# Kernel optimization log

Measured on AMD Instinct MI355X. Metric: run time of the kernel, lower is better.

Reference implementation:

```python
import jax, jax.numpy as jnp
import numpy as np

WS = 11        # gaussian window size
SIGMA = 1.5    # gaussian sigma
L = 10.0       # val_range
SSIM_C1 = (0.01 * L) ** 2
SSIM_C2 = (0.03 * L) ** 2


def _window():
    g = jnp.exp(-((jnp.arange(WS) - WS // 2) ** 2) / (2.0 * SIGMA ** 2))
    g = g / g.sum()
    return jnp.outer(g, g).astype(jnp.float32)  # [11,11], sums to 1


def _blur(z, win):
    # depthwise 11x11 gaussian blur with VALID padding; z: [..., H, W]
    lead = z.shape[:-2]
    zf = z.reshape((-1, 1) + z.shape[-2:])
    out = jax.lax.conv_general_dilated(zf, win[None, None], (1, 1), 'VALID')
    return out.reshape(lead + out.shape[-2:])


def setup_inputs() -> dict:
    key = jax.random.key(0)
    ks = jax.random.split(key, 7)
    B, C, Fc, H, W = 8, 64, 3, 192, 192
    return {
        'x': jax.random.normal(ks[0], (B, C, H, W), jnp.float32),
        'x_feature': jax.random.normal(ks[1], (B, Fc, H, W), jnp.float32),
        'spatial_w': jax.random.normal(ks[2], (1, Fc, 3, 1), jnp.float32) * 0.1,
        'W1': jax.random.normal(ks[3], (C, C), jnp.float32) * 0.05,
        'b1': jnp.zeros((C,), jnp.float32),
        'W2': jax.random.normal(ks[4], (C, C), jnp.float32) * 0.05,
        'b2': jnp.zeros((C,), jnp.float32),
    }


def reference(x, x_feature, spatial_w, W1, b1, W2, b2):
    win = _window()
    # per-channel gaussian moments (computed once, reused across all pairs)
    mu_x = _blur(x, win)                         # [B,C,h,w]
    mu_f = _blur(x_feature, win)                 # [B,F,h,w]
    sig_x = _blur(x * x, win) - mu_x ** 2        # variance of x channels
    sig_f = _blur(x_feature * x_feature, win) - mu_f ** 2
    # all pairwise cross-covariances in one batched blur
    prod = x_feature[:, :, None] * x[:, None]    # [B,F,C,H,W]
    sig_fx = _blur(prod, win) - mu_f[:, :, None] * mu_x[:, None]
    v1 = 2.0 * sig_fx + SSIM_C2
    v2 = sig_f[:, :, None] + sig_x[:, None] + SSIM_C2
    num = (2.0 * mu_f[:, :, None] * mu_x[:, None] + SSIM_C1) * v1
    den = (mu_f[:, :, None] ** 2 + mu_x[:, None] ** 2 + SSIM_C1) * v2
    ssim_info = (num / den).mean(axis=(-2, -1))  # [B,F,C]
    # spatial gate: Conv2d(3,1,(3,1),padding=(1,0)) over [B,F,C,1]
    si4 = ssim_info[..., None]                   # [B,F,C,1]
    h = jax.lax.conv_general_dilated(si4, spatial_w, (1, 1), ((1, 1), (0, 0)))
    h = jax.nn.relu(h).reshape(x.shape[0], -1)   # [B,C]
    h = jax.nn.relu(h @ W1.T + b1) @ W2.T + b2
    return jax.nn.sigmoid(h), ssim_info
```

## Files before the change

kernel.cpp:

```cpp
#include <hip/hip_runtime.h>
#include <math.h>

#define HW 192
#define OW 182
#define NPIX (OW*OW)
#define SSIM_C1 0.01f
#define SSIM_C2 0.09f

#define Gk0 0.0010283835f
#define Gk1 0.0075987615f
#define Gk2 0.0360007700f
#define Gk3 0.1093608000f
#define Gk4 0.2130055400f
#define Gk5 0.2660117000f

typedef float v2f __attribute__((ext_vector_type(2)));

__device__ __forceinline__ v2f vfma(float w, v2f a, v2f b) {
    return __builtin_elementwise_fma((v2f){w, w}, a, b);
}
__device__ __forceinline__ v2f vfma2(v2f w, v2f a, v2f b) {
    return __builtin_elementwise_fma(w, a, b);
}

__device__ __forceinline__ void dgauss(float g[11]) {
    float s = 0.f;
#pragma unroll
    for (int i = 0; i < 11; ++i) {
        float d = (float)(i - 5);
        g[i] = expf(-(d * d) / 4.5f);
        s += g[i];
    }
    float inv = 1.f / s;
#pragma unroll
    for (int i = 0; i < 11; ++i) g[i] *= inv;
}

__global__ __launch_bounds__(256) void muf_kernel(const float* __restrict__ xf,
                                                  float* __restrict__ muf,
                                                  float* __restrict__ sigc2f) {
    const int tile = blockIdx.x % 14;
    const int img  = blockIdx.x / 14;
    const int r0   = tile * 13;

    __shared__ float raw[23][192];
    __shared__ float hb[2][23][184];

    float g[11]; dgauss(g);
    const int t = threadIdx.x;
    const float* src = xf + (size_t)img * HW * HW;

    for (int i = t; i < 23 * 192; i += 256) {
        int rr = i / 192, col = i - rr * 192;
        raw[rr][col] = src[(r0 + rr) * HW + col];
    }
    __syncthreads();

    for (int i = t; i < 23 * OW; i += 256) {
        int rr = i / OW, co = i - rr * OW;
        float a0 = 0.f, a1 = 0.f;
#pragma unroll
        for (int k = 0; k < 11; ++k) {
            float v = raw[rr][co + k];
            float w = g[k];
            a0 += w * v;
            a1 += w * v * v;
        }
        hb[0][rr][co] = a0;
        hb[1][rr][co] = a1;
    }
    __syncthreads();

    for (int i = t; i < 13 * OW; i += 256) {
        int rr = i / OW, co = i - rr * OW;
        float m = 0.f, s2 = 0.f;
#pragma unroll
        for (int k = 0; k < 11; ++k) {
            float w = g[k];
            m  += w * hb[0][rr + k][co];
            s2 += w * hb[1][rr + k][co];
        }
        size_t o = (size_t)img * NPIX + (size_t)(r0 + rr) * OW + co;
        muf[o]    = m;
        sigc2f[o] = s2 - m * m + SSIM_C2;
    }
}

__global__ __launch_bounds__(192, 4) void ssim_kernel(const float* __restrict__ x,
                                                      const float* __restrict__ xf,
                                                      const float* __restrict__ muf,
                                                      const float* __restrict__ sigc2f,
                                                      float* __restrict__ part) {
    const float G[11] = {Gk0,Gk1,Gk2,Gk3,Gk4,Gk5,Gk4,Gk3,Gk2,Gk1,Gk0};
    const v2f WA[6] = {{G[0],0.f},{G[2],G[1]},{G[4],G[3]},{G[6],G[5]},{G[8],G[7]},{G[10],G[9]}};
    const v2f WB[6] = {{G[1],G[0]},{G[3],G[2]},{G[5],G[4]},{G[7],G[6]},{G[9],G[8]},{0.f,G[10]}};

    const int blk  = blockIdx.x;
    const int c    = blk & 63;
    const int tile = (blk >> 6) & 3;
    const int b    = blk >> 8;

    const int out0  = (tile * 182) >> 2;
    const int out1  = ((tile + 1) * 182) >> 2;
    const int n_out = out1 - out0;

    const int t    = threadIdx.x;
    const int half = (t >= 96) ? 1 : 0;
    const int u    = half ? (t - 96) : t;
    const int cu   = 2 * u;
    const bool act = (u <= 90);

    const float* xp  = x  + ((size_t)(b * 64 + c)) * HW * HW + (size_t)out0 * HW + t;
    const float* fp0 = xf + ((size_t)(b * 3 + 0)) * HW * HW + (size_t)out0 * HW + t;
    const float* fp1 = fp0 + HW * HW;
    const float* fp2 = fp1 + HW * HW;

    const float* mp = muf    + (size_t)(b * 3) * NPIX + (size_t)(out0 + half) * OW + cu;
    const float* cp = sigc2f + (size_t)(b * 3) * NPIX + (size_t)(out0 + half) * OW + cu;

    __shared__ float eb[4][5][192];
    __shared__ float red[3][3];

    v2f P01[10], P23[10];
    float P4[10];
#pragma unroll
    for (int j = 0; j < 10; ++j) { P01[j] = (v2f){0.f,0.f}; P23[j] = (v2f){0.f,0.f}; P4[j] = 0.f; }

    v2f A0 = {0.f,0.f}, A1 = {0.f,0.f}, A2 = {0.f,0.f};

    v2f eE01, eE23; float eE4;

    auto vstep = [&](float xv, float a0, float a1, float a2, bool emit) {
        v2f v01 = {xv, xv * xv};
        v2f v23 = {xv * a0, xv * a1};
        float v4 = xv * a2;
        if (emit) {
            eE01 = vfma(G[10], v01, P01[0]);
            eE23 = vfma(G[10], v23, P23[0]);
            eE4  = fmaf(G[10], v4, P4[0]);
        }
#pragma unroll
        for (int j = 0; j < 9; ++j) {
            P01[j] = vfma(G[9 - j], v01, P01[j + 1]);
            P23[j] = vfma(G[9 - j], v23, P23[j + 1]);
            P4[j]  = fmaf(G[9 - j], v4, P4[j + 1]);
        }
        P01[9] = G[0] * v01;
        P23[9] = G[0] * v23;
        P4[9]  = G[0] * v4;
    };

#pragma unroll 1
    for (int r = 0; r < 10; r += 2) {
        float xA = xp[0],  aA0 = fp0[0],  aA1 = fp1[0],  aA2 = fp2[0];
        float xB = xp[HW], aB0 = fp0[HW], aB1 = fp1[HW], aB2 = fp2[HW];
        xp += 2 * HW; fp0 += 2 * HW; fp1 += 2 * HW; fp2 += 2 * HW;
        vstep(xA, aA0, aA1, aA2, false);
        vstep(xB, aB0, aB1, aB2, false);
    }

    const int n_pair = n_out >> 1;
#pragma unroll 1
    for (int p = 0; p < n_pair; ++p) {
        const int e = 2 * p;
        float xA = xp[0],  aA0 = fp0[0],  aA1 = fp1[0],  aA2 = fp2[0];
        float xB = xp[HW], aB0 = fp0[HW], aB1 = fp1[HW], aB2 = fp2[HW];
        xp += 2 * HW; fp0 += 2 * HW; fp1 += 2 * HW; fp2 += 2 * HW;

        v2f mf0, mf1, mf2, cc0, cc1, cc2;
        if (act) {
            mf0 = *(const v2f*)(mp);
            mf1 = *(const v2f*)(mp + NPIX);
            mf2 = *(const v2f*)(mp + 2 * NPIX);
            cc0 = *(const v2f*)(cp);
            cc1 = *(const v2f*)(cp + NPIX);
            cc2 = *(const v2f*)(cp + 2 * NPIX);
            mp += 2 * OW; cp += 2 * OW;
        }

        const int sA = e & 3, sB = (e + 1) & 3;
        vstep(xA, aA0, aA1, aA2, true);
        eb[sA][0][t] = eE01.x; eb[sA][1][t] = eE01.y;
        eb[sA][2][t] = eE23.x; eb[sA][3][t] = eE23.y;
        eb[sA][4][t] = eE4;
        vstep(xB, aB0, aB1, aB2, true);
        eb[sB][0][t] = eE01.x; eb[sB][1][t] = eE01.y;
        eb[sB][2][t] = eE23.x; eb[sB][3][t] = eE23.y;
        eb[sB][4][t] = eE4;
        __syncthreads();

        if (act) {
            const int sH = half ? sB : sA;
            v2f h0, h1, h2, h3, h4;
            {
                v2f hacc[5];
#pragma unroll
                for (int f = 0; f < 5; ++f) {
                    const float* ep = &eb[sH][f][cu];
                    v2f a = {0.f, 0.f};
#pragma unroll
                    for (int m = 0; m < 6; ++m) {
                        v2f rd = *(const v2f*)(ep + 2 * m);
                        a = vfma2(WA[m], __builtin_shufflevector(rd, rd, 0, 0), a);
                        a = vfma2(WB[m], __builtin_shufflevector(rd, rd, 1, 1), a);
                    }
                    hacc[f] = a;
                }
                h0 = hacc[0]; h1 = hacc[1]; h2 = hacc[2]; h3 = hacc[3]; h4 = hacc[4];
            }
            const v2f mux  = h0;
            const v2f mux2 = mux * mux;
            const v2f sigc = h1 - mux2;
            {
                v2f t1  = mf0 * mux;
                v2f sfx = h2 - t1;
                v2f v1s = vfma(2.f, sfx, (v2f){SSIM_C2, SSIM_C2});
                v2f n1  = vfma(2.f, t1, (v2f){SSIM_C1, SSIM_C1});
                v2f num = n1 * v1s;
                v2f qd  = vfma2(mf0, mf0, (v2f){SSIM_C1, SSIM_C1});
                v2f den = (qd + mux2) * (cc0 + sigc);
                v2f inv = {__builtin_amdgcn_rcpf(den.x), __builtin_amdgcn_rcpf(den.y)};
                A0 = vfma2(num, inv, A0);
            }
            {
                v2f t1  = mf1 * mux;
                v2f sfx = h3 - t1;
                v2f v1s = vfma(2.f, sfx, (v2f){SSIM_C2, SSIM_C2});
                v2f n1  = vfma(2.f, t1, (v2f){SSIM_C1, SSIM_C1});
                v2f num = n1 * v1s;
                v2f qd  = vfma2(mf1, mf1, (v2f){SSIM_C1, SSIM_C1});
                v2f den = (qd + mux2) * (cc1 + sigc);
                v2f inv = {__builtin_amdgcn_rcpf(den.x), __builtin_amdgcn_rcpf(den.y)};
                A1 = vfma2(num, inv, A1);
            }
            {
                v2f t1  = mf2 * mux;
                v2f sfx = h4 - t1;
                v2f v1s = vfma(2.f, sfx, (v2f){SSIM_C2, SSIM_C2});
                v2f n1  = vfma(2.f, t1, (v2f){SSIM_C1, SSIM_C1});
                v2f num = n1 * v1s;
                v2f qd  = vfma2(mf2, mf2, (v2f){SSIM_C1, SSIM_C1});
                v2f den = (qd + mux2) * (cc2 + sigc);
                v2f inv = {__builtin_amdgcn_rcpf(den.x), __builtin_amdgcn_rcpf(den.y)};
                A2 = vfma2(num, inv, A2);
            }
        }
    }

    if (n_out & 1) {
        const int e = n_out - 1;
        float xA = xp[0], aA0 = fp0[0], aA1 = fp1[0], aA2 = fp2[0];
        vstep(xA, aA0, aA1, aA2, true);
        const int sA = e & 3;
        eb[sA][0][t] = eE01.x; eb[sA][1][t] = eE01.y;
        eb[sA][2][t] = eE23.x; eb[sA][3][t] = eE23.y;
        eb[sA][4][t] = eE4;
        __syncthreads();
        if (act && half == 0) {
            v2f mf0 = *(const v2f*)(mp);
            v2f mf1 = *(const v2f*)(mp + NPIX);
            v2f mf2 = *(const v2f*)(mp + 2 * NPIX);
            v2f cc0 = *(const v2f*)(cp);
            v2f cc1 = *(const v2f*)(cp + NPIX);
            v2f cc2 = *(const v2f*)(cp + 2 * NPIX);
            v2f hacc[5];
#pragma unroll
            for (int f = 0; f < 5; ++f) {
                const float* ep = &eb[sA][f][cu];
                v2f a = {0.f, 0.f};
#pragma unroll
                for (int m = 0; m < 6; ++m) {
                    v2f rd = *(const v2f*)(ep + 2 * m);
                    a = vfma2(WA[m], __builtin_shufflevector(rd, rd, 0, 0), a);
                    a = vfma2(WB[m], __builtin_shufflevector(rd, rd, 1, 1), a);
                }
                hacc[f] = a;
            }
            const v2f mux  = hacc[0];
            const v2f mux2 = mux * mux;
            const v2f sigc = hacc[1] - mux2;
            {
                v2f t1  = mf0 * mux;
                v2f sfx = hacc[2] - t1;
                v2f v1s = vfma(2.f, sfx, (v2f){SSIM_C2, SSIM_C2});
                v2f n1  = vfma(2.f, t1, (v2f){SSIM_C1, SSIM_C1});
                v2f num = n1 * v1s;
                v2f qd  = vfma2(mf0, mf0, (v2f){SSIM_C1, SSIM_C1});
                v2f den = (qd + mux2) * (cc0 + sigc);
                v2f inv = {__builtin_amdgcn_rcpf(den.x), __builtin_amdgcn_rcpf(den.y)};
                A0 = vfma2(num, inv, A0);
            }
            {
                v2f t1  = mf1 * mux;
                v2f sfx = hacc[3] - t1;
                v2f v1s = vfma(2.f, sfx, (v2f){SSIM_C2, SSIM_C2});
                v2f n1  = vfma(2.f, t1, (v2f){SSIM_C1, SSIM_C1});
                v2f num = n1 * v1s;
                v2f qd  = vfma2(mf1, mf1, (v2f){SSIM_C1, SSIM_C1});
                v2f den = (qd + mux2) * (cc1 + sigc);
                v2f inv = {__builtin_amdgcn_rcpf(den.x), __builtin_amdgcn_rcpf(den.y)};
                A1 = vfma2(num, inv, A1);
            }
            {
                v2f t1  = mf2 * mux;
                v2f sfx = hacc[4] - t1;
                v2f v1s = vfma(2.f, sfx, (v2f){SSIM_C2, SSIM_C2});
                v2f n1  = vfma(2.f, t1, (v2f){SSIM_C1, SSIM_C1});
                v2f num = n1 * v1s;
                v2f qd  = vfma2(mf2, mf2, (v2f){SSIM_C1, SSIM_C1});
                v2f den = (qd + mux2) * (cc2 + sigc);
                v2f inv = {__builtin_amdgcn_rcpf(den.x), __builtin_amdgcn_rcpf(den.y)};
                A2 = vfma2(num, inv, A2);
            }
        }
    }

    float acc0 = A0.x + A0.y;
    float acc1 = A1.x + A1.y;
    float acc2 = A2.x + A2.y;
#pragma unroll
    for (int off = 32; off > 0; off >>= 1) {
        acc0 += __shfl_down(acc0, off);
        acc1 += __shfl_down(acc1, off);
        acc2 += __shfl_down(acc2, off);
    }
    const int wid = t >> 6, lane = t & 63;
    if (lane == 0) { red[0][wid] = acc0; red[1][wid] = acc1; red[2][wid] = acc2; }
    __syncthreads();
    if (t == 0) {
        const size_t o = (size_t)tile * 1536 + (size_t)b * 192;
        part[o +   0 + c] = red[0][0] + red[0][1] + red[0][2];
        part[o +  64 + c] = red[1][0] + red[1][1] + red[1][2];
        part[o + 128 + c] = red[2][0] + red[2][1] + red[2][2];
    }
}

__global__ __launch_bounds__(64) void gate_kernel(const float* __restrict__ part,
                                                  const float* __restrict__ sw,
                                                  const float* __restrict__ W1,
                                                  const float* __restrict__ b1,
                                                  const float* __restrict__ W2,
                                                  const float* __restrict__ b2,
                                                  float* __restrict__ out,
                                                  float* __restrict__ out_ssim) {
    const int b = blockIdx.x;
    const int c = threadIdx.x;

    __shared__ float s[3][64];
    __shared__ float h0[64];
    __shared__ float h1[64];

    const float inv = 1.f / (float)NPIX;
#pragma unroll
    for (int f = 0; f < 3; ++f) {
        const int i = b * 192 + f * 64 + c;
        float v = (part[i] + part[1536 + i]) + (part[3072 + i] + part[4608 + i]);
        v *= inv;
        s[f][c] = v;
        out_ssim[i] = v;
    }
    __syncthreads();

    float a = 0.f;
#pragma unroll
    for (int f = 0; f < 3; ++f)
#pragma unroll
        for (int i = 0; i < 3; ++i) {
            int cc = c - 1 + i;
            if (cc >= 0 && cc < 64) a += sw[f * 3 + i] * s[f][cc];
        }
    h0[c] = fmaxf(a, 0.f);
    __syncthreads();

    float a1 = b1[c];
    for (int j = 0; j < 64; ++j) a1 += W1[c * 64 + j] * h0[j];
    h1[c] = fmaxf(a1, 0.f);
    __syncthreads();

    float a2 = b2[c];
    for (int j = 0; j < 64; ++j) a2 += W2[c * 64 + j] * h1[j];
    out[b * 64 + c] = 1.f / (1.f + expf(-a2));
}

extern "C" void kernel_launch(void* const* d_in, const int* in_sizes, int n_in,
                              void* d_out, int out_size, void* d_ws, size_t ws_size,
                              hipStream_t stream) {
    const float* x  = (const float*)d_in[0];
    const float* xf = (const float*)d_in[1];
    const float* sw = (const float*)d_in[2];
    const float* W1 = (const float*)d_in[3];
    const float* b1 = (const float*)d_in[4];
    const float* W2 = (const float*)d_in[5];
    const float* b2 = (const float*)d_in[6];
    float* out = (float*)d_out;

    float* muf  = (float*)d_ws;
    float* sigf = muf + 24 * NPIX;
    float* part = sigf + 24 * NPIX;

    muf_kernel <<<24 * 14, 256, 0, stream>>>(xf, muf, sigf);
    ssim_kernel<<<2048,    192, 0, stream>>>(x, xf, muf, sigf, part);
    gate_kernel<<<8,        64, 0, stream>>>(part, sw, W1, b1, W2, b2, out, out + 512);
}
```

Baseline: 112.1 us.

## Split rows into eight tiles and software-prefetch next input rows

Doubles the number of row tiles per image channel (4 to 8), so 4096 blocks are launched and the gate kernel sums eight partials. The main loop now loads the next pair of input rows before processing the current pair, hiding global load latency behind the blur and SSIM math. Eight tiles means each block recomputes the 10-row vertical warm-up over fewer output rows, which adds redundant reads and FMAs. The SSIM epilogue is also folded into a lambda for readability.

Result: faster. 108.5 us (-3.2%).

```diff
diff --git a/kernel.cpp b/kernel.cpp
--- a/kernel.cpp
+++ b/kernel.cpp
@@ -4,6 +4,7 @@
 #define HW 192
 #define OW 182
 #define NPIX (OW*OW)
+#define NTILE 8
 #define SSIM_C1 0.01f
 #define SSIM_C2 0.09f
 
@@ -97,11 +98,11 @@
 
     const int blk  = blockIdx.x;
     const int c    = blk & 63;
-    const int tile = (blk >> 6) & 3;
-    const int b    = blk >> 8;
-
-    const int out0  = (tile * 182) >> 2;
-    const int out1  = ((tile + 1) * 182) >> 2;
+    const int tile = (blk >> 6) & 7;
+    const int b    = blk >> 9;
+
+    const int out0  = (tile * 182) >> 3;
+    const int out1  = ((tile + 1) * 182) >> 3;
     const int n_out = out1 - out0;
 
     const int t    = threadIdx.x;
@@ -150,6 +151,20 @@
         P4[9]  = G[0] * v4;
     };
 
+    auto ssim2 = [&](const v2f mux, const v2f sigc,
+                     const v2f mf, const v2f cc, const v2f h, v2f& A) {
+        const v2f mux2 = mux * mux;
+        v2f t1  = mf * mux;
+        v2f sfx = h - t1;
+        v2f v1s = vfma(2.f, sfx, (v2f){SSIM_C2, SSIM_C2});
+        v2f n1  = vfma(2.f, t1, (v2f){SSIM_C1, SSIM_C1});
+        v2f num = n1 * v1s;
+        v2f qd  = vfma2(mf, mf, (v2f){SSIM_C1, SSIM_C1});
+        v2f den = (qd + mux2) * (cc + sigc);
+        v2f inv = {__builtin_amdgcn_rcpf(den.x), __builtin_amdgcn_rcpf(den.y)};
+        A = vfma2(num, inv, A);
+    };
+
 #pragma unroll 1
     for (int r = 0; r < 10; r += 2) {
         float xA = xp[0],  aA0 = fp0[0],  aA1 = fp1[0],  aA2 = fp2[0];
@@ -160,12 +175,18 @@
     }
 
     const int n_pair = n_out >> 1;
+
+    float xA = xp[0],  aA0 = fp0[0],  aA1 = fp1[0],  aA2 = fp2[0];
+    float xB = xp[HW], aB0 = fp0[HW], aB1 = fp1[HW], aB2 = fp2[HW];
+
 #pragma unroll 1
     for (int p = 0; p < n_pair; ++p) {
-        const int e = 2 * p;
-        float xA = xp[0],  aA0 = fp0[0],  aA1 = fp1[0],  aA2 = fp2[0];
-        float xB = xp[HW], aB0 = fp0[HW], aB1 = fp1[HW], aB2 = fp2[HW];
-        xp += 2 * HW; fp0 += 2 * HW; fp1 += 2 * HW; fp2 += 2 * HW;
+        const int rb = 2 * (p + 1);
+        const int r1 = (rb     < n_out) ? rb     : (n_out - 1);
+        const int r2 = (rb + 1 < n_out) ? rb + 1 : (n_out - 1);
+        const int o1 = r1 * HW, o2 = r2 * HW;
+        const float nxA = xp[o1], naA0 = fp0[o1], naA1 = fp1[o1], naA2 = fp2[o1];
+        const float nxB = xp[o2], naB0 = fp0[o2], naB1 = fp1[o2], naB2 = fp2[o2];
 
         v2f mf0, mf1, mf2, cc0, cc1, cc2;
         if (act) {
@@ -178,6 +199,7 @@
             mp += 2 * OW; cp += 2 * OW;
         }
 
+        const int e = 2 * p;
         const int sA = e & 3, sB = (e + 1) & 3;
         vstep(xA, aA0, aA1, aA2, true);
         eb[sA][0][t] = eE01.x; eb[sA][1][t] = eE01.y;
@@ -189,67 +211,34 @@
         eb[sB][4][t] = eE4;
         __syncthreads();
 
+        xA = nxA; aA0 = naA0; aA1 = naA1; aA2 = naA2;
+        xB = nxB; aB0 = naB0; aB1 = naB1; aB2 = naB2;
+
         if (act) {
             const int sH = half ? sB : sA;
-            v2f h0, h1, h2, h3, h4;
-            {
-                v2f hacc[5];
-#pragma unroll
-                for (int f = 0; f < 5; ++f) {
-                    const float* ep = &eb[sH][f][cu];
-                    v2f a = {0.f, 0.f};
-#pragma unroll
-                    for (int m = 0; m < 6; ++m) {
-                        v2f rd = *(const v2f*)(ep + 2 * m);
-                        a = vfma2(WA[m], __builtin_shufflevector(rd, rd, 0, 0), a);
-                        a = vfma2(WB[m], __builtin_shufflevector(rd, rd, 1, 1), a);
-                    }
-                    hacc[f] = a;
+            v2f hacc[5];
+#pragma unroll
+            for (int f = 0; f < 5; ++f) {
+                const float* ep = &eb[sH][f][cu];
+                v2f a = {0.f, 0.f};
+#pragma unroll
+                for (int m = 0; m < 6; ++m) {
+                    v2f rd = *(const v2f*)(ep + 2 * m);
+                    a = vfma2(WA[m], __builtin_shufflevector(rd, rd, 0, 0), a);
+                    a = vfma2(WB[m], __builtin_shufflevector(rd, rd, 1, 1), a);
                 }
-                h0 = hacc[0]; h1 = hacc[1]; h2 = hacc[2]; h3 = hacc[3]; h4 = hacc[4];
+                hacc[f] = a;
             }
-            const v2f mux  = h0;
-            const v2f mux2 = mux * mux;
-            const v2f sigc = h1 - mux2;
-            {
-                v2f t1  = mf0 * mux;
-                v2f sfx = h2 - t1;
-                v2f v1s = vfma(2.f, sfx, (v2f){SSIM_C2, SSIM_C2});
-                v2f n1  = vfma(2.f, t1, (v2f){SSIM_C1, SSIM_C1});
-                v2f num = n1 * v1s;
-                v2f qd  = vfma2(mf0, mf0, (v2f){SSIM_C1, SSIM_C1});
-                v2f den = (qd + mux2) * (cc0 + sigc);
-                v2f inv = {__builtin_amdgcn_rcpf(den.x), __builtin_amdgcn_rcpf(den.y)};
-                A0 = vfma2(num, inv, A0);
-            }
-            {
-                v2f t1  = mf1 * mux;
-                v2f sfx = h3 - t1;
-                v2f v1s = vfma(2.f, sfx, (v2f){SSIM_C2, SSIM_C2});
-                v2f n1  = vfma(2.f, t1, (v2f){SSIM_C1, SSIM_C1});
-                v2f num = n1 * v1s;
-                v2f qd  = vfma2(mf1, mf1, (v2f){SSIM_C1, SSIM_C1});
-                v2f den = (qd + mux2) * (cc1 + sigc);
-                v2f inv = {__builtin_amdgcn_rcpf(den.x), __builtin_amdgcn_rcpf(den.y)};
-                A1 = vfma2(num, inv, A1);
-            }
-            {
-                v2f t1  = mf2 * mux;
-                v2f sfx = h4 - t1;
-                v2f v1s = vfma(2.f, sfx, (v2f){SSIM_C2, SSIM_C2});
-                v2f n1  = vfma(2.f, t1, (v2f){SSIM_C1, SSIM_C1});
-                v2f num = n1 * v1s;
-                v2f qd  = vfma2(mf2, mf2, (v2f){SSIM_C1, SSIM_C1});
-                v2f den = (qd + mux2) * (cc2 + sigc);
-                v2f inv = {__builtin_amdgcn_rcpf(den.x), __builtin_amdgcn_rcpf(den.y)};
-                A2 = vfma2(num, inv, A2);
-            }
+            const v2f mux  = hacc[0];
+            const v2f sigc = hacc[1] - mux * mux;
+            ssim2(mux, sigc, mf0, cc0, hacc[2], A0);
+            ssim2(mux, sigc, mf1, cc1, hacc[3], A1);
+            ssim2(mux, sigc, mf2, cc2, hacc[4], A2);
         }
     }
 
     if (n_out & 1) {
         const int e = n_out - 1;
-        float xA = xp[0], aA0 = fp0[0], aA1 = fp1[0], aA2 = fp2[0];
         vstep(xA, aA0, aA1, aA2, true);
         const int sA = e & 3;
         eb[sA][0][t] = eE01.x; eb[sA][1][t] = eE01.y;
@@ -277,41 +266,10 @@
                 hacc[f] = a;
             }
             const v2f mux  = hacc[0];
-            const v2f mux2 = mux * mux;
-            const v2f sigc = hacc[1] - mux2;
-            {
-                v2f t1  = mf0 * mux;
-                v2f sfx = hacc[2] - t1;
-                v2f v1s = vfma(2.f, sfx, (v2f){SSIM_C2, SSIM_C2});
-                v2f n1  = vfma(2.f, t1, (v2f){SSIM_C1, SSIM_C1});
-                v2f num = n1 * v1s;
-                v2f qd  = vfma2(mf0, mf0, (v2f){SSIM_C1, SSIM_C1});
-                v2f den = (qd + mux2) * (cc0 + sigc);
-                v2f inv = {__builtin_amdgcn_rcpf(den.x), __builtin_amdgcn_rcpf(den.y)};
-                A0 = vfma2(num, inv, A0);
-            }
-            {
-                v2f t1  = mf1 * mux;
-                v2f sfx = hacc[3] - t1;
-                v2f v1s = vfma(2.f, sfx, (v2f){SSIM_C2, SSIM_C2});
-                v2f n1  = vfma(2.f, t1, (v2f){SSIM_C1, SSIM_C1});
-                v2f num = n1 * v1s;
-                v2f qd  = vfma2(mf1, mf1, (v2f){SSIM_C1, SSIM_C1});
-                v2f den = (qd + mux2) * (cc1 + sigc);
-                v2f inv = {__builtin_amdgcn_rcpf(den.x), __builtin_amdgcn_rcpf(den.y)};
-                A1 = vfma2(num, inv, A1);
-            }
-            {
-                v2f t1  = mf2 * mux;
-                v2f sfx = hacc[4] - t1;
-                v2f v1s = vfma(2.f, sfx, (v2f){SSIM_C2, SSIM_C2});
-                v2f n1  = vfma(2.f, t1, (v2f){SSIM_C1, SSIM_C1});
-                v2f num = n1 * v1s;
-                v2f qd  = vfma2(mf2, mf2, (v2f){SSIM_C1, SSIM_C1});
-                v2f den = (qd + mux2) * (cc2 + sigc);
-                v2f inv = {__builtin_amdgcn_rcpf(den.x), __builtin_amdgcn_rcpf(den.y)};
-                A2 = vfma2(num, inv, A2);
-            }
+            const v2f sigc = hacc[1] - mux * mux;
+            ssim2(mux, sigc, mf0, cc0, hacc[2], A0);
+            ssim2(mux, sigc, mf1, cc1, hacc[3], A1);
+            ssim2(mux, sigc, mf2, cc2, hacc[4], A2);
         }
     }
 
@@ -354,7 +312,9 @@
 #pragma unroll
     for (int f = 0; f < 3; ++f) {
         const int i = b * 192 + f * 64 + c;
-        float v = (part[i] + part[1536 + i]) + (part[3072 + i] + part[4608 + i]);
+        float v = 0.f;
+#pragma unroll
+        for (int k = 0; k < NTILE; ++k) v += part[i + k * 1536];
         v *= inv;
         s[f][c] = v;
         out_ssim[i] = v;
@@ -398,7 +358,7 @@
     float* sigf = muf + 24 * NPIX;
     float* part = sigf + 24 * NPIX;
 
-    muf_kernel <<<24 * 14, 256, 0, stream>>>(xf, muf, sigf);
-    ssim_kernel<<<2048,    192, 0, stream>>>(x, xf, muf, sigf, part);
-    gate_kernel<<<8,        64, 0, stream>>>(part, sw, W1, b1, W2, b2, out, out + 512);
-}
+    muf_kernel <<<24 * 14,        256, 0, stream>>>(xf, muf, sigf);
+    ssim_kernel<<<8 * 64 * NTILE, 192, 0, stream>>>(x, xf, muf, sigf, part);
+    gate_kernel<<<8,               64, 0, stream>>>(part, sw, W1, b1, W2, b2, out, out + 512);
+}
```
